# Kernel tuning notes

Hardware: AMD Instinct MI355X
Metric: run time of the kernel (lower is better)

The kernel has to match this reference:

```python
import jax, jax.numpy as jnp
import numpy as np

BATCH, MAX_LEN, LEN_FORBIDDEN = 256, 512, 1024


def setup_inputs() -> dict:
    key = jax.random.key(0)
    kA, kB = jax.random.split(key)
    A = jax.random.normal(kA, (BATCH, MAX_LEN, 2), dtype=jnp.float32)
    B = jax.random.normal(kB, (2, LEN_FORBIDDEN), dtype=jnp.float32)
    return {"A": A, "B": B}


def reference(A, B):
    batch, L, _ = A.shape
    F = B.shape[1]
    # Pairwise broadcast subtract: (b, L, 2, 1) - (1, 1, 2, F) -> (b, L, 2, F)
    C = A[:, :, :, None] - B[None, None, :, :]
    # Two-sided sigmoid 'bump': peaks at 0.25 when C == 0
    bump = jax.nn.sigmoid(10.0 * C) * jax.nn.sigmoid(-10.0 * C)
    # split([1,1], axis=2) + keras minimum -> elementwise min over the coord axis
    m = jnp.minimum(bump[:, :, 0, :], bump[:, :, 1, :])  # (b, L, F)
    # Faithful raw Reshape((1, F, L)) — this MIXES the L and F axes (row-major
    # relabeling, NOT a transpose), exactly as tf.keras.layers.Reshape does.
    r = m.reshape(batch, 1, F, L)  # (b, H=1, W=F, C=L)
    # MaxPooling2D(pool_size=(1, F), strides=1, 'valid') == max over the W axis
    pooled = jnp.max(r, axis=2)  # (b, 1, L)
    # Reshape((-1,)) then global reduce_min over axis=1, keepdims
    return jnp.min(pooled.reshape(batch, -1), axis=1, keepdims=True)  # (b, 1)
```

## Files before the change

### kernel.cpp

```cpp
#include <hip/hip_runtime.h>

constexpr int BATCH  = 256;
constexpr int MAXLEN = 512;
constexpr int LENF   = 1024;

__global__ __launch_bounds__(512)
void chebbump_kernel(const float* __restrict__ A,
                     const float* __restrict__ B,
                     float* __restrict__ out)
{
    const int b = blockIdx.x;
    const int c = threadIdx.x;

    const float* __restrict__ Ab = A + (size_t)b * (MAXLEN * 2);

    const float b0c = B[c];
    const float b1c = B[LENF + c];
    const float b0d = B[c + MAXLEN];
    const float b1d = B[LENF + MAXLEN + c];

    float u0 = 3.4e38f, u1 = 3.4e38f, u2 = 3.4e38f, u3 = 3.4e38f;
#pragma unroll 4
    for (int l = 0; l < MAXLEN; l += 4) {
        const float a00 = Ab[2 * l + 0], a10 = Ab[2 * l + 1];
        const float a01 = Ab[2 * l + 2], a11 = Ab[2 * l + 3];
        const float a02 = Ab[2 * l + 4], a12 = Ab[2 * l + 5];
        const float a03 = Ab[2 * l + 6], a13 = Ab[2 * l + 7];
        u0 = fminf(u0, fminf(fmaxf(fabsf(a00 - b0c), fabsf(a10 - b1c)),
                             fmaxf(fabsf(a00 - b0d), fabsf(a10 - b1d))));
        u1 = fminf(u1, fminf(fmaxf(fabsf(a01 - b0c), fabsf(a11 - b1c)),
                             fmaxf(fabsf(a01 - b0d), fabsf(a11 - b1d))));
        u2 = fminf(u2, fminf(fmaxf(fabsf(a02 - b0c), fabsf(a12 - b1c)),
                             fmaxf(fabsf(a02 - b0d), fabsf(a12 - b1d))));
        u3 = fminf(u3, fminf(fmaxf(fabsf(a03 - b0c), fabsf(a13 - b1c)),
                             fmaxf(fabsf(a03 - b0d), fabsf(a13 - b1d))));
    }
    float v = fminf(fminf(u0, u1), fminf(u2, u3));

    __shared__ float sw[8];
#pragma unroll
    for (int off = 32; off > 0; off >>= 1)
        v = fmaxf(v, __shfl_xor(v, off));
    if ((c & 63) == 0) sw[c >> 6] = v;
    __syncthreads();

    if (c == 0) {
        float t = sw[0];
#pragma unroll
        for (int i = 1; i < 8; ++i) t = fmaxf(t, sw[i]);
        const float e = expf(-10.0f * t);
        const float d = 1.0f + e;
        out[b] = e / (d * d);
    }
}

extern "C" void kernel_launch(void* const* d_in, const int* in_sizes, int n_in,
                              void* d_out, int out_size, void* d_ws, size_t ws_size,
                              hipStream_t stream)
{
    const float* A = (const float*)d_in[0];
    const float* B = (const float*)d_in[1];
    float* out = (float*)d_out;

    hipLaunchKernelGGL(chebbump_kernel, dim3(BATCH), dim3(512), 0, stream,
                       A, B, out);
}
```

Measured before the change: 19.41 us.

## Split L loop across four blocks per batch and combine in second kernel

Splits the per-batch loop over MAXLEN into four quarter blocks, so the first kernel launches 1024 blocks instead of 256. Each block writes its per-channel minima to workspace, and a second kernel combines the four partials and does the max reduction and sigmoid bump. The aim is better occupancy across the GPU's compute units. The cost is an extra kernel launch and a global-memory round trip for the partial results.

```diff
diff --git a/kernel.cpp b/kernel.cpp
--- a/kernel.cpp
+++ b/kernel.cpp
@@ -3,25 +3,29 @@
 constexpr int BATCH  = 256;
 constexpr int MAXLEN = 512;
 constexpr int LENF   = 1024;
+constexpr int NQ     = 4;
+constexpr int LQ     = MAXLEN / NQ;
 
 __global__ __launch_bounds__(512)
-void chebbump_kernel(const float* __restrict__ A,
-                     const float* __restrict__ B,
-                     float* __restrict__ out)
+void chebmin_part_kernel(const float* __restrict__ A,
+                         const float* __restrict__ B,
+                         float* __restrict__ part)
 {
-    const int b = blockIdx.x;
-    const int c = threadIdx.x;
+    const int bid = blockIdx.x;
+    const int b   = bid >> 2;
+    const int q   = bid & 3;
+    const int c   = threadIdx.x;
 
-    const float* __restrict__ Ab = A + (size_t)b * (MAXLEN * 2);
+    const float* __restrict__ Ab = A + (size_t)b * (MAXLEN * 2) + q * (LQ * 2);
 
     const float b0c = B[c];
     const float b1c = B[LENF + c];
-    const float b0d = B[c + MAXLEN];
+    const float b0d = B[MAXLEN + c];
     const float b1d = B[LENF + MAXLEN + c];
 
     float u0 = 3.4e38f, u1 = 3.4e38f, u2 = 3.4e38f, u3 = 3.4e38f;
 #pragma unroll 4
-    for (int l = 0; l < MAXLEN; l += 4) {
+    for (int l = 0; l < LQ; l += 4) {
         const float a00 = Ab[2 * l + 0], a10 = Ab[2 * l + 1];
         const float a01 = Ab[2 * l + 2], a11 = Ab[2 * l + 3];
         const float a02 = Ab[2 * l + 4], a12 = Ab[2 * l + 5];
@@ -35,7 +39,20 @@
         u3 = fminf(u3, fminf(fmaxf(fabsf(a03 - b0c), fabsf(a13 - b1c)),
                              fmaxf(fabsf(a03 - b0d), fabsf(a13 - b1d))));
     }
-    float v = fminf(fminf(u0, u1), fminf(u2, u3));
+
+    part[(size_t)bid * MAXLEN + c] = fminf(fminf(u0, u1), fminf(u2, u3));
+}
+
+__global__ __launch_bounds__(512)
+void combine_bump_kernel(const float* __restrict__ part,
+                         float* __restrict__ out)
+{
+    const int b = blockIdx.x;
+    const int c = threadIdx.x;
+    const float* __restrict__ p = part + (size_t)b * (NQ * MAXLEN);
+
+    float v = fminf(fminf(p[c], p[MAXLEN + c]),
+                    fminf(p[2 * MAXLEN + c], p[3 * MAXLEN + c]));
 
     __shared__ float sw[8];
 #pragma unroll
@@ -45,10 +62,10 @@
     __syncthreads();
 
     if (c == 0) {
-        float t = sw[0];
+        float m = sw[0];
 #pragma unroll
-        for (int i = 1; i < 8; ++i) t = fmaxf(t, sw[i]);
-        const float e = expf(-10.0f * t);
+        for (int i = 1; i < 8; ++i) m = fmaxf(m, sw[i]);
+        const float e = expf(-10.0f * m);
         const float d = 1.0f + e;
         out[b] = e / (d * d);
     }
@@ -60,8 +77,11 @@
 {
     const float* A = (const float*)d_in[0];
     const float* B = (const float*)d_in[1];
-    float* out = (float*)d_out;
+    float* out  = (float*)d_out;
+    float* part = (float*)d_ws;
 
-    hipLaunchKernelGGL(chebbump_kernel, dim3(BATCH), dim3(512), 0, stream,
-                       A, B, out);
+    hipLaunchKernelGGL(chebmin_part_kernel, dim3(BATCH * NQ), dim3(512), 0, stream,
+                       A, B, part);
+    hipLaunchKernelGGL(combine_bump_kernel, dim3(BATCH), dim3(512), 0, stream,
+                       part, out);
 }
```

Result: faster. 18.37 us (-5.4%).
